# Kernel optimization log

Measured on AMD Instinct MI355X. Metric: run time of the kernel, lower is better.

The kernel has to match this reference:

```python
import jax, jax.numpy as jnp
import numpy as np

N_NODES = 100000
N_EDGES = 1600000
N_GRAPHS = 2000
N_VALUES = 10000
EMB_DIM = 256
N_FEATS = 4


def setup_inputs() -> dict:
    key = jax.random.key(0)
    ks = jax.random.split(key, 7)
    feature = jax.random.randint(ks[0], (N_NODES, N_FEATS), 0, N_VALUES)
    src = jax.random.randint(ks[1], (N_EDGES,), 0, N_NODES)
    dst = jax.random.randint(ks[2], (N_EDGES,), 0, N_NODES)
    graph_ids = jnp.sort(jax.random.randint(ks[3], (N_NODES,), 0, N_GRAPHS))
    emb_table = jax.random.normal(ks[4], (N_VALUES, EMB_DIM), dtype=jnp.float32) * 0.1
    W1 = jax.random.normal(ks[5], (EMB_DIM, EMB_DIM), dtype=jnp.float32) * (EMB_DIM ** -0.5)
    W2 = jax.random.normal(ks[6], (EMB_DIM, EMB_DIM), dtype=jnp.float32) * (EMB_DIM ** -0.5)
    return {"feature": feature, "src": src, "dst": dst, "graph_ids": graph_ids,
            "emb_table": emb_table, "W1": W1, "W2": W2}


def _degree_norms(src, dst, n_nodes):
    ones = jnp.ones(src.shape[0], dtype=jnp.float32)
    out_deg = jax.ops.segment_sum(ones, src, num_segments=n_nodes)
    in_deg = jax.ops.segment_sum(ones, dst, num_segments=n_nodes)
    out_norm = jnp.where(out_deg > 0, jax.lax.rsqrt(jnp.maximum(out_deg, 1.0)), 0.0)[:, None]
    in_norm = jnp.where(in_deg > 0, jax.lax.rsqrt(jnp.maximum(in_deg, 1.0)), 0.0)[:, None]
    return out_norm, in_norm


def _gcn_layer(h, src, dst, out_norm, in_norm, W=None):
    # DGL GraphConv, norm='both', no bias: D_out^{-1/2} scaling, (optional) weight,
    # copy-src/sum aggregation, D_in^{-1/2} scaling.
    h = h * out_norm
    if W is not None:
        h = h @ W
    agg = jax.ops.segment_sum(h[src], dst, num_segments=h.shape[0])  # [N, D]
    return agg * in_norm


def reference(feature, src, dst, graph_ids, emb_table, W1, W2):
    # Embedding lookup + sum over per-node feature slots: [N, F, D] -> [N, D]
    h = jnp.sum(emb_table[feature], axis=1)
    out_norm, in_norm = _degree_norms(src, dst, h.shape[0])
    # layer 0: weight=False
    h = _gcn_layer(h, src, dst, out_norm, in_norm, W=None)
    h = jax.nn.relu(h)
    # layer 1: with weight
    h = _gcn_layer(h, src, dst, out_norm, in_norm, W=W1)
    h = jax.nn.relu(h)
    # final layer: with weight, no relu
    h = _gcn_layer(h, src, dst, out_norm, in_norm, W=W2)
    # sum pooling per graph
    graph_embedding = jax.ops.segment_sum(h, graph_ids, num_segments=N_GRAPHS)
    return graph_embedding
```

## Files before the change

### kernel.cpp

```cpp
#include <hip/hip_runtime.h>
#include <hip/hip_fp16.h>

#define NN 100000
#define NE 1600000
#define NG 2000
#define DIM 256
#define NF 4
#define SCAN_B 1024
#define NBLK ((NN + SCAN_B - 1) / SCAN_B)
#define SCAT_BLK 2048
#define WCONV_BLK 128
#define EMB_BLK ((NN * 64) / 256)

using half8 = __attribute__((ext_vector_type(8))) _Float16;
using f32x4 = __attribute__((ext_vector_type(4))) float;

__device__ inline float4 h4_to_f4(uint2 v) {
    __half2 a = *reinterpret_cast<__half2*>(&v.x);
    __half2 b = *reinterpret_cast<__half2*>(&v.y);
    float2 fa = __half22float2(a);
    float2 fb = __half22float2(b);
    return make_float4(fa.x, fa.y, fb.x, fb.y);
}

__device__ inline uint2 f4_to_h4(float4 r) {
    __half2 a = __floats2half2_rn(r.x, r.y);
    __half2 b = __floats2half2_rn(r.z, r.w);
    uint2 o;
    o.x = *reinterpret_cast<uint*>(&a);
    o.y = *reinterpret_cast<uint*>(&b);
    return o;
}

__device__ inline void add8(float4& a0, float4& a1, uint4 u) {
    uint2 lo2; lo2.x = u.x; lo2.y = u.y;
    uint2 hi2; hi2.x = u.z; hi2.y = u.w;
    float4 lo = h4_to_f4(lo2);
    float4 hi = h4_to_f4(hi2);
    a0.x += lo.x; a0.y += lo.y; a0.z += lo.z; a0.w += lo.w;
    a1.x += hi.x; a1.y += hi.y; a1.z += hi.z; a1.w += hi.w;
}

__global__ void k_count(const int* __restrict__ src, const int* __restrict__ dst,
                        int* __restrict__ outd, int* __restrict__ ind,
                        ushort* __restrict__ slots) {
    int i = blockIdx.x * blockDim.x + threadIdx.x;
    int stride = gridDim.x * blockDim.x;
    for (; i < NE; i += stride) {
        atomicAdd(&outd[src[i]], 1);
        int s = atomicAdd(&ind[dst[i]], 1);
        slots[i] = (ushort)s;
    }
}

__global__ __launch_bounds__(1024) void k_scan1(const int* __restrict__ deg,
                                                int* __restrict__ locex,
                                                int* __restrict__ partials) {
    __shared__ int sm[SCAN_B];
    int t = threadIdx.x;
    int i = blockIdx.x * SCAN_B + t;
    int v = (i < NN) ? deg[i] : 0;
    sm[t] = v;
    __syncthreads();
    for (int off = 1; off < SCAN_B; off <<= 1) {
        int u = (t >= off) ? sm[t - off] : 0;
        __syncthreads();
        sm[t] += u;
        __syncthreads();
    }
    if (i < NN) locex[i] = sm[t] - v;
    if (t == SCAN_B - 1) partials[blockIdx.x] = sm[t];
}

__global__ __launch_bounds__(128) void k_scan2(int* __restrict__ partials,
                                               int* __restrict__ rowptr_last) {
    __shared__ int sm[128];
    int t = threadIdx.x;
    int v = (t < NBLK) ? partials[t] : 0;
    sm[t] = v;
    __syncthreads();
    for (int off = 1; off < 128; off <<= 1) {
        int u = (t >= off) ? sm[t - off] : 0;
        __syncthreads();
        sm[t] += u;
        __syncthreads();
    }
    if (t < NBLK) partials[t] = sm[t] - v;
    if (t == 127) *rowptr_last = sm[127];
}

__global__ __launch_bounds__(1024) void k_scan3(const int* __restrict__ locex,
                                                const int* __restrict__ partials,
                                                const int* __restrict__ outd,
                                                const int* __restrict__ ind,
                                                int* __restrict__ rowptr,
                                                float* __restrict__ onorm,
                                                float* __restrict__ inorm) {
    int i = blockIdx.x * SCAN_B + threadIdx.x;
    if (i < NN) {
        rowptr[i] = locex[i] + partials[blockIdx.x];
        int od = outd[i];
        int id = ind[i];
        onorm[i] = od > 0 ? rsqrtf((float)od) : 0.f;
        inorm[i] = id > 0 ? rsqrtf((float)id) : 0.f;
    }
}

__global__ void k_scatter_wconv_embed(const int* __restrict__ src, const int* __restrict__ dst,
                                      const int* __restrict__ rowptr,
                                      const ushort* __restrict__ slots,
                                      int* __restrict__ col,
                                      const float* __restrict__ W1,
                                      ushort* __restrict__ Wt1,
                                      const int* __restrict__ feat, const float* __restrict__ emb,
                                      const float* __restrict__ onorm, ushort* __restrict__ h) {
    int tid = threadIdx.x;
    if (blockIdx.x < SCAT_BLK) {
        int i = blockIdx.x * 256 + tid;
        const int stride = SCAT_BLK * 256;
        for (; i < NE; i += stride) {
            int d = dst[i];
            col[rowptr[d] + (int)slots[i]] = src[i];
        }
    } else if (blockIdx.x < SCAT_BLK + WCONV_BLK) {
        int idx = (blockIdx.x - SCAT_BLK) * 512 + tid * 2;
        int k0 = idx >> 8;
        int n0 = idx & 255;
        reinterpret_cast<__fp16*>(Wt1)[n0 * DIM + k0] = (__fp16)W1[idx];
        int idx1 = idx + 1;
        int k1 = idx1 >> 8;
        int n1 = idx1 & 255;
        reinterpret_cast<__fp16*>(Wt1)[n1 * DIM + k1] = (__fp16)W1[idx1];
    } else {
        int idx = (blockIdx.x - SCAT_BLK - WCONV_BLK) * 256 + tid;
        int node = idx >> 6;
        int g = idx & 63;
        if (node >= NN) return;
        const int4 f = *reinterpret_cast<const int4*>(feat + node * 4);
        const float4* emb4 = reinterpret_cast<const float4*>(emb);
        float4 a = emb4[(long)f.x * 64 + g];
        float4 b = emb4[(long)f.y * 64 + g];
        float4 c = emb4[(long)f.z * 64 + g];
        float4 d = emb4[(long)f.w * 64 + g];
        float sc = onorm[node];
        float4 r;
        r.x = (a.x + b.x + c.x + d.x) * sc;
        r.y = (a.y + b.y + c.y + d.y) * sc;
        r.z = (a.z + b.z + c.z + d.z) * sc;
        r.w = (a.w + b.w + c.w + d.w) * sc;
        reinterpret_cast<uint2*>(h)[(long)node * 64 + g] = f4_to_h4(r);
    }
}

template <int MODE>
__global__ void k_agg(const int* __restrict__ rowptr, const int* __restrict__ col,
                      const ushort* __restrict__ hin, const float* __restrict__ inorm,
                      const float* __restrict__ onorm, ushort* __restrict__ hout) {
    int wid = (blockIdx.x * blockDim.x + threadIdx.x) >> 6;
    int lane = threadIdx.x & 63;
    if (wid >= NN) return;
    int half = lane >> 5;
    int l32 = lane & 31;
    int e0 = rowptr[wid];
    int e1 = rowptr[wid + 1];
    const uint4* hin4 = reinterpret_cast<const uint4*>(hin);
    float4 aA0 = {0,0,0,0}, aA1 = {0,0,0,0};
    float4 aB0 = {0,0,0,0}, aB1 = {0,0,0,0};
    int e = e0;
    for (; e + 8 <= e1; e += 8) {
        int s0 = col[e + 0 + half];
        int s1 = col[e + 2 + half];
        int s2 = col[e + 4 + half];
        int s3 = col[e + 6 + half];
        uint4 u0 = hin4[(long)s0 * 32 + l32];
        uint4 u1 = hin4[(long)s1 * 32 + l32];
        uint4 u2 = hin4[(long)s2 * 32 + l32];
        uint4 u3 = hin4[(long)s3 * 32 + l32];
        add8(aA0, aA1, u0);
        add8(aB0, aB1, u1);
        add8(aA0, aA1, u2);
        add8(aB0, aB1, u3);
    }
    for (; e < e1; e += 2) {
        int idx = e + half;
        if (idx < e1) {
            int s = col[idx];
            uint4 u = hin4[(long)s * 32 + l32];
            add8(aA0, aA1, u);
        }
    }
    float f[8];
    f[0] = aA0.x + aB0.x; f[1] = aA0.y + aB0.y; f[2] = aA0.z + aB0.z; f[3] = aA0.w + aB0.w;
    f[4] = aA1.x + aB1.x; f[5] = aA1.y + aB1.y; f[6] = aA1.z + aB1.z; f[7] = aA1.w + aB1.w;
#pragma unroll
    for (int j = 0; j < 8; ++j) f[j] += __shfl_xor(f[j], 32);

    float sc = inorm[wid];
    float4 r0, r1;
    if (MODE == 0) {
        float on = onorm[wid];
        r0.x = fmaxf(f[0] * sc, 0.f) * on;
        r0.y = fmaxf(f[1] * sc, 0.f) * on;
        r0.z = fmaxf(f[2] * sc, 0.f) * on;
        r0.w = fmaxf(f[3] * sc, 0.f) * on;
        r1.x = fmaxf(f[4] * sc, 0.f) * on;
        r1.y = fmaxf(f[5] * sc, 0.f) * on;
        r1.z = fmaxf(f[6] * sc, 0.f) * on;
        r1.w = fmaxf(f[7] * sc, 0.f) * on;
    } else {
        r0.x = f[0] * sc; r0.y = f[1] * sc; r0.z = f[2] * sc; r0.w = f[3] * sc;
        r1.x = f[4] * sc; r1.y = f[5] * sc; r1.z = f[6] * sc; r1.w = f[7] * sc;
    }
    if (half == 0) {
        uint2 lo = f4_to_h4(r0);
        uint2 hi = f4_to_h4(r1);
        uint4 o; o.x = lo.x; o.y = lo.y; o.z = hi.x; o.w = hi.y;
        reinterpret_cast<uint4*>(hout)[(long)wid * 32 + l32] = o;
    }
}

__global__ __launch_bounds__(512, 2) void k_gemm(const ushort* __restrict__ x,
                                                 const ushort* __restrict__ Wt,
                                                 ushort* __restrict__ y) {
    __shared__ char wl[131072];
    int tid = threadIdx.x;
    const uint4* Wt4 = reinterpret_cast<const uint4*>(Wt);
#pragma unroll
    for (int it = 0; it < 16; ++it) {
        int chunk = it * 512 + tid;
        int n = chunk >> 5;
        int c16 = chunk & 31;
        uint4 v = Wt4[chunk];
        int off = ((n << 9) + (c16 << 4)) ^ ((n & 7) << 4);
        *reinterpret_cast<uint4*>(&wl[off]) = v;
    }
    __syncthreads();

    int w = tid >> 6;
    int l = tid & 63;
    int wrow = blockIdx.x * 384 + w * 48;
    int lrow = l & 15;
    int lk = l >> 4;

    f32x4 acc[3][16];
#pragma unroll
    for (int m = 0; m < 3; ++m)
#pragma unroll
        for (int n = 0; n < 16; ++n) acc[m][n] = {0.f, 0.f, 0.f, 0.f};

    const char* xb = reinterpret_cast<const char*>(x);
    int r0 = wrow + lrow;
    int r1 = r0 + 16;
    int r2 = r0 + 32;
    r0 = r0 < NN ? r0 : NN - 1;
    r1 = r1 < NN ? r1 : NN - 1;
    r2 = r2 < NN ? r2 : NN - 1;

#pragma unroll
    for (int ks = 0; ks < DIM; ks += 32) {
        long kbyte = (long)(ks + lk * 8) * 2;
        half8 a0 = *reinterpret_cast<const half8*>(xb + (long)r0 * 512 + kbyte);
        half8 a1 = *reinterpret_cast<const half8*>(xb + (long)r1 * 512 + kbyte);
        half8 a2 = *reinterpret_cast<const half8*>(xb + (long)r2 * 512 + kbyte);
#pragma unroll
        for (int fn = 0; fn < 16; ++fn) {
            int n = fn * 16 + lrow;
            int off = ((n << 9) + (int)kbyte) ^ ((n & 7) << 4);
            half8 b = *reinterpret_cast<const half8*>(&wl[off]);
            acc[0][fn] = __builtin_amdgcn_mfma_f32_16x16x32_f16(a0, b, acc[0][fn], 0, 0, 0);
            acc[1][fn] = __builtin_amdgcn_mfma_f32_16x16x32_f16(a1, b, acc[1][fn], 0, 0, 0);
            acc[2][fn] = __builtin_amdgcn_mfma_f32_16x16x32_f16(a2, b, acc[2][fn], 0, 0, 0);
        }
    }

    __fp16* yh = reinterpret_cast<__fp16*>(y);
#pragma unroll
    for (int m = 0; m < 3; ++m) {
        int rbase = wrow + m * 16 + lk * 4;
#pragma unroll
        for (int fn = 0; fn < 16; ++fn) {
            int colc = fn * 16 + lrow;
#pragma unroll
            for (int r = 0; r < 4; ++r) {
                int row = rbase + r;
                if (row < NN) yh[(long)row * DIM + colc] = (__fp16)acc[m][fn][r];
            }
        }
    }
}

__device__ inline int lbound(const int* __restrict__ a, int n, int v) {
    int lo = 0, hi = n;
    while (lo < hi) {
        int m = (lo + hi) >> 1;
        if (a[m] < v) lo = m + 1; else hi = m;
    }
    return lo;
}

__global__ __launch_bounds__(256) void k_pool(const ushort* __restrict__ h,
                                              const int* __restrict__ gids,
                                              float* __restrict__ P) {
    int g = blockIdx.x;
    int t = threadIdx.x;
    int lo = lbound(gids, NN, g);
    int hi = lbound(gids, NN, g + 1);
    const __fp16* hh = reinterpret_cast<const __fp16*>(h);
    float acc = 0.f;
    for (int nd = lo; nd < hi; ++nd) acc += (float)hh[(long)nd * DIM + t];
    P[(long)g * DIM + t] = acc;
}

__global__ __launch_bounds__(256) void k_pgemm(const float* __restrict__ P,
                                               const float* __restrict__ W2,
                                               float* __restrict__ out) {
    __shared__ float Pl[8][DIM];
    int t = threadIdx.x;
    int rbase = blockIdx.x * 8;
#pragma unroll
    for (int r = 0; r < 8; ++r) Pl[r][t] = P[(long)(rbase + r) * DIM + t];
    __syncthreads();
    float acc[8];
#pragma unroll
    for (int r = 0; r < 8; ++r) acc[r] = 0.f;
    for (int k = 0; k < DIM; ++k) {
        float w = W2[(long)k * DIM + t];
#pragma unroll
        for (int r = 0; r < 8; ++r) acc[r] += Pl[r][k] * w;
    }
#pragma unroll
    for (int r = 0; r < 8; ++r) out[(long)(rbase + r) * DIM + t] = acc[r];
}

extern "C" void kernel_launch(void* const* d_in, const int* in_sizes, int n_in,
                              void* d_out, int out_size, void* d_ws, size_t ws_size,
                              hipStream_t stream) {
    const int* feature = (const int*)d_in[0];
    const int* src = (const int*)d_in[1];
    const int* dst = (const int*)d_in[2];
    const int* gids = (const int*)d_in[3];
    const float* emb = (const float*)d_in[4];
    const float* W1 = (const float*)d_in[5];
    const float* W2 = (const float*)d_in[6];
    float* out = (float*)d_out;

    char* p = (char*)d_ws;
    ushort* hA = (ushort*)p;            p += (size_t)NN * DIM * 2;
    ushort* hB = (ushort*)p;            p += (size_t)NN * DIM * 2;
    ushort* Wt1 = (ushort*)p;           p += (size_t)DIM * DIM * 2;
    float* onorm = (float*)p;           p += (size_t)NN * 4;
    float* inorm = (float*)p;           p += (size_t)NN * 4;
    int* rowptr = (int*)p;              p += (size_t)(NN + 4) * 4;
    int* colidx = (int*)p;              p += (size_t)NE * 4;
    int* outd = (int*)p;                p += (size_t)NN * 4;
    int* ind = (int*)p;                 p += (size_t)NN * 4;
    int* locex = (int*)p;               p += (size_t)NN * 4;
    int* partials = (int*)p;            p += (size_t)128 * 4;
    ushort* slots = (ushort*)p;         p += (size_t)NE * 2;
    float* Pbuf = (float*)p;            p += (size_t)NG * DIM * 4;

    hipMemsetAsync(outd, 0, (size_t)2 * NN * 4, stream);

    k_count<<<2048, 256, 0, stream>>>(src, dst, outd, ind, slots);
    k_scan1<<<NBLK, SCAN_B, 0, stream>>>(ind, locex, partials);
    k_scan2<<<1, 128, 0, stream>>>(partials, rowptr + NN);
    k_scan3<<<NBLK, SCAN_B, 0, stream>>>(locex, partials, outd, ind, rowptr, onorm, inorm);
    k_scatter_wconv_embed<<<SCAT_BLK + WCONV_BLK + EMB_BLK, 256, 0, stream>>>(
        src, dst, rowptr, slots, colidx, W1, Wt1, feature, emb, onorm, hA);

    const int aggGrid = (NN * 64 + 255) / 256;
    const int gemmGrid = (NN + 383) / 384;
    k_agg<0><<<aggGrid, 256, 0, stream>>>(rowptr, colidx, hA, inorm, onorm, hB);
    k_gemm<<<gemmGrid, 512, 0, stream>>>(hB, Wt1, hA);
    k_agg<0><<<aggGrid, 256, 0, stream>>>(rowptr, colidx, hA, inorm, onorm, hB);
    k_agg<1><<<aggGrid, 256, 0, stream>>>(rowptr, colidx, hB, inorm, onorm, hA);
    k_pool<<<NG, 256, 0, stream>>>(hA, gids, Pbuf);
    k_pgemm<<<NG / 8, 256, 0, stream>>>(Pbuf, W2, out);
}
```

Baseline: 637.6 us.

## Build CSR via two-level bucket sort instead of global atomic counting

Replaces the per-edge global atomic in-degree counting, the three-kernel scan and the slot-based scatter with a bucketed counting sort. Edges are first binned into 196 coarse destination buckets using shared-memory histograms, then each bucket is sorted locally in LDS to produce rowptr, col and inorm. The out-norm computation is folded into the embedding kernel, which removes two kernel launches. The aim is to cut contended global atomics and random global writes. The cost is an extra 8-byte pair buffer pass, and the sort falls back to direct global writes when a bucket overflows LDS.

After: 577.5 us. 1.1x faster.

```diff
diff --git a/kernel.cpp b/kernel.cpp
--- a/kernel.cpp
+++ b/kernel.cpp
@@ -6,11 +6,16 @@
 #define NG 2000
 #define DIM 256
 #define NF 4
-#define SCAN_B 1024
-#define NBLK ((NN + SCAN_B - 1) / SCAN_B)
-#define SCAT_BLK 2048
+#define NBUK 196
+#define BSH 9
+#define BNODES 512
+#define CHUNKS 512
+#define CHUNK_E (NE / CHUNKS)
+#define OUTD_BLK 1024
+#define BH_BLK CHUNKS
 #define WCONV_BLK 128
 #define EMB_BLK ((NN * 64) / 256)
+#define COLBUF_CAP 12288
 
 using half8 = __attribute__((ext_vector_type(8))) _Float16;
 using f32x4 = __attribute__((ext_vector_type(4))) float;
@@ -41,114 +46,169 @@
     a1.x += hi.x; a1.y += hi.y; a1.z += hi.z; a1.w += hi.w;
 }
 
-__global__ void k_count(const int* __restrict__ src, const int* __restrict__ dst,
-                        int* __restrict__ outd, int* __restrict__ ind,
-                        ushort* __restrict__ slots) {
-    int i = blockIdx.x * blockDim.x + threadIdx.x;
-    int stride = gridDim.x * blockDim.x;
-    for (; i < NE; i += stride) {
-        atomicAdd(&outd[src[i]], 1);
-        int s = atomicAdd(&ind[dst[i]], 1);
-        slots[i] = (ushort)s;
-    }
-}
-
-__global__ __launch_bounds__(1024) void k_scan1(const int* __restrict__ deg,
-                                                int* __restrict__ locex,
-                                                int* __restrict__ partials) {
-    __shared__ int sm[SCAN_B];
-    int t = threadIdx.x;
-    int i = blockIdx.x * SCAN_B + t;
-    int v = (i < NN) ? deg[i] : 0;
-    sm[t] = v;
-    __syncthreads();
-    for (int off = 1; off < SCAN_B; off <<= 1) {
-        int u = (t >= off) ? sm[t - off] : 0;
-        __syncthreads();
-        sm[t] += u;
-        __syncthreads();
-    }
-    if (i < NN) locex[i] = sm[t] - v;
-    if (t == SCAN_B - 1) partials[blockIdx.x] = sm[t];
-}
-
-__global__ __launch_bounds__(128) void k_scan2(int* __restrict__ partials,
-                                               int* __restrict__ rowptr_last) {
-    __shared__ int sm[128];
-    int t = threadIdx.x;
-    int v = (t < NBLK) ? partials[t] : 0;
-    sm[t] = v;
-    __syncthreads();
-    for (int off = 1; off < 128; off <<= 1) {
-        int u = (t >= off) ? sm[t - off] : 0;
-        __syncthreads();
-        sm[t] += u;
-        __syncthreads();
-    }
-    if (t < NBLK) partials[t] = sm[t] - v;
-    if (t == 127) *rowptr_last = sm[127];
-}
-
-__global__ __launch_bounds__(1024) void k_scan3(const int* __restrict__ locex,
-                                                const int* __restrict__ partials,
-                                                const int* __restrict__ outd,
-                                                const int* __restrict__ ind,
-                                                int* __restrict__ rowptr,
-                                                float* __restrict__ onorm,
-                                                float* __restrict__ inorm) {
-    int i = blockIdx.x * SCAN_B + threadIdx.x;
-    if (i < NN) {
-        rowptr[i] = locex[i] + partials[blockIdx.x];
-        int od = outd[i];
-        int id = ind[i];
-        onorm[i] = od > 0 ? rsqrtf((float)od) : 0.f;
-        inorm[i] = id > 0 ? rsqrtf((float)id) : 0.f;
-    }
-}
-
-__global__ void k_scatter_wconv_embed(const int* __restrict__ src, const int* __restrict__ dst,
-                                      const int* __restrict__ rowptr,
-                                      const ushort* __restrict__ slots,
-                                      int* __restrict__ col,
-                                      const float* __restrict__ W1,
-                                      ushort* __restrict__ Wt1,
-                                      const int* __restrict__ feat, const float* __restrict__ emb,
-                                      const float* __restrict__ onorm, ushort* __restrict__ h) {
+__global__ void k_hist(const int* __restrict__ src, const int* __restrict__ dst,
+                       int* __restrict__ outd, int* __restrict__ bcnt,
+                       const float* __restrict__ W1, ushort* __restrict__ Wt1) {
     int tid = threadIdx.x;
-    if (blockIdx.x < SCAT_BLK) {
+    if (blockIdx.x < OUTD_BLK) {
         int i = blockIdx.x * 256 + tid;
-        const int stride = SCAT_BLK * 256;
-        for (; i < NE; i += stride) {
-            int d = dst[i];
-            col[rowptr[d] + (int)slots[i]] = src[i];
-        }
-    } else if (blockIdx.x < SCAT_BLK + WCONV_BLK) {
-        int idx = (blockIdx.x - SCAT_BLK) * 512 + tid * 2;
-        int k0 = idx >> 8;
-        int n0 = idx & 255;
+        const int stride = OUTD_BLK * 256;
+        for (; i < NE; i += stride) atomicAdd(&outd[src[i]], 1);
+    } else if (blockIdx.x < OUTD_BLK + BH_BLK) {
+        __shared__ int h[NBUK];
+        int cb = blockIdx.x - OUTD_BLK;
+        int e0 = cb * CHUNK_E;
+        if (tid < NBUK) h[tid] = 0;
+        __syncthreads();
+        for (int e = e0 + tid; e < e0 + CHUNK_E; e += 256)
+            atomicAdd(&h[dst[e] >> BSH], 1);
+        __syncthreads();
+        if (tid < NBUK && h[tid] > 0) atomicAdd(&bcnt[tid], h[tid]);
+    } else {
+        int idx = (blockIdx.x - OUTD_BLK - BH_BLK) * 512 + tid * 2;
+        int k0 = idx >> 8, n0 = idx & 255;
         reinterpret_cast<__fp16*>(Wt1)[n0 * DIM + k0] = (__fp16)W1[idx];
         int idx1 = idx + 1;
-        int k1 = idx1 >> 8;
-        int n1 = idx1 & 255;
+        int k1 = idx1 >> 8, n1 = idx1 & 255;
         reinterpret_cast<__fp16*>(Wt1)[n1 * DIM + k1] = (__fp16)W1[idx1];
+    }
+}
+
+__global__ __launch_bounds__(256) void k_bscan(const int* __restrict__ bcnt,
+                                               int* __restrict__ boff,
+                                               int* __restrict__ gcur) {
+    __shared__ int sm[256];
+    int t = threadIdx.x;
+    int v = (t < NBUK) ? bcnt[t] : 0;
+    sm[t] = v;
+    __syncthreads();
+    for (int off = 1; off < 256; off <<= 1) {
+        int u = (t >= off) ? sm[t - off] : 0;
+        __syncthreads();
+        sm[t] += u;
+        __syncthreads();
+    }
+    if (t < NBUK) {
+        int ex = sm[t] - v;
+        boff[t] = ex;
+        gcur[t] = ex;
+    }
+    if (t == 255) boff[NBUK] = sm[255];
+}
+
+__global__ void k_bscatter_embed(const int* __restrict__ src, const int* __restrict__ dst,
+                                 int* __restrict__ gcur, uint2* __restrict__ pairs,
+                                 const int* __restrict__ feat, const float* __restrict__ emb,
+                                 const int* __restrict__ outd,
+                                 float* __restrict__ onorm, ushort* __restrict__ h) {
+    int tid = threadIdx.x;
+    if (blockIdx.x < CHUNKS) {
+        __shared__ int h1[NBUK];
+        __shared__ int base1[NBUK];
+        __shared__ int cur1[NBUK];
+        int e0 = blockIdx.x * CHUNK_E;
+        if (tid < NBUK) h1[tid] = 0;
+        __syncthreads();
+        for (int e = e0 + tid; e < e0 + CHUNK_E; e += 256)
+            atomicAdd(&h1[dst[e] >> BSH], 1);
+        __syncthreads();
+        if (tid < NBUK) {
+            int c = h1[tid];
+            base1[tid] = (c > 0) ? atomicAdd(&gcur[tid], c) : 0;
+            cur1[tid] = 0;
+        }
+        __syncthreads();
+        for (int e = e0 + tid; e < e0 + CHUNK_E; e += 256) {
+            int d = dst[e];
+            int b = d >> BSH;
+            int r = atomicAdd(&cur1[b], 1);
+            uint2 pr;
+            pr.x = (uint)d;
+            pr.y = (uint)src[e];
+            pairs[base1[b] + r] = pr;
+        }
     } else {
-        int idx = (blockIdx.x - SCAT_BLK - WCONV_BLK) * 256 + tid;
+        int idx = (blockIdx.x - CHUNKS) * 256 + tid;
         int node = idx >> 6;
         int g = idx & 63;
         if (node >= NN) return;
+        int od = outd[node];
+        float sc = od > 0 ? rsqrtf((float)od) : 0.f;
+        if (g == 0) onorm[node] = sc;
         const int4 f = *reinterpret_cast<const int4*>(feat + node * 4);
         const float4* emb4 = reinterpret_cast<const float4*>(emb);
         float4 a = emb4[(long)f.x * 64 + g];
         float4 b = emb4[(long)f.y * 64 + g];
         float4 c = emb4[(long)f.z * 64 + g];
         float4 d = emb4[(long)f.w * 64 + g];
-        float sc = onorm[node];
         float4 r;
         r.x = (a.x + b.x + c.x + d.x) * sc;
         r.y = (a.y + b.y + c.y + d.y) * sc;
         r.z = (a.z + b.z + c.z + d.z) * sc;
         r.w = (a.w + b.w + c.w + d.w) * sc;
         reinterpret_cast<uint2*>(h)[(long)node * 64 + g] = f4_to_h4(r);
+    }
+}
+
+__global__ __launch_bounds__(1024) void k_bsort(const uint2* __restrict__ pairs,
+                                                const int* __restrict__ boff,
+                                                int* __restrict__ col,
+                                                int* __restrict__ rowptr,
+                                                float* __restrict__ inorm) {
+    __shared__ int hist[BNODES];
+    __shared__ int sc[BNODES];
+    __shared__ int ex[BNODES];
+    __shared__ int cur[BNODES];
+    __shared__ int colbuf[COLBUF_CAP];
+    int t = threadIdx.x;
+    int b = blockIdx.x;
+    int o0 = boff[b];
+    int n = boff[b + 1] - o0;
+
+    if (t < BNODES) hist[t] = 0;
+    __syncthreads();
+    for (int i = t; i < n; i += 1024) {
+        uint2 p = pairs[o0 + i];
+        atomicAdd(&hist[p.x & (BNODES - 1)], 1);
+    }
+    __syncthreads();
+    int v = (t < BNODES) ? hist[t] : 0;
+    if (t < BNODES) sc[t] = v;
+    __syncthreads();
+    for (int off = 1; off < BNODES; off <<= 1) {
+        int u = (t < BNODES && t >= off) ? sc[t - off] : 0;
+        __syncthreads();
+        if (t < BNODES) sc[t] += u;
+        __syncthreads();
+    }
+    if (t < BNODES) {
+        ex[t] = sc[t] - v;
+        cur[t] = 0;
+        int node = (b << BSH) + t;
+        if (node < NN) {
+            rowptr[node] = o0 + ex[t];
+            inorm[node] = v > 0 ? rsqrtf((float)v) : 0.f;
+        }
+    }
+    if (b == NBUK - 1 && t == 0) rowptr[NN] = NE;
+    __syncthreads();
+
+    if (n <= COLBUF_CAP) {
+        for (int i = t; i < n; i += 1024) {
+            uint2 p = pairs[o0 + i];
+            int ld = p.x & (BNODES - 1);
+            int r = atomicAdd(&cur[ld], 1);
+            colbuf[ex[ld] + r] = (int)p.y;
+        }
+        __syncthreads();
+        for (int i = t; i < n; i += 1024) col[o0 + i] = colbuf[i];
+    } else {
+        for (int i = t; i < n; i += 1024) {
+            uint2 p = pairs[o0 + i];
+            int ld = p.x & (BNODES - 1);
+            int r = atomicAdd(&cur[ld], 1);
+            col[o0 + ex[ld] + r] = (int)p.y;
+        }
     }
 }
 
@@ -195,21 +255,21 @@
 #pragma unroll
     for (int j = 0; j < 8; ++j) f[j] += __shfl_xor(f[j], 32);
 
-    float sc = inorm[wid];
+    float scn = inorm[wid];
     float4 r0, r1;
     if (MODE == 0) {
         float on = onorm[wid];
-        r0.x = fmaxf(f[0] * sc, 0.f) * on;
-        r0.y = fmaxf(f[1] * sc, 0.f) * on;
-        r0.z = fmaxf(f[2] * sc, 0.f) * on;
-        r0.w = fmaxf(f[3] * sc, 0.f) * on;
-        r1.x = fmaxf(f[4] * sc, 0.f) * on;
-        r1.y = fmaxf(f[5] * sc, 0.f) * on;
-        r1.z = fmaxf(f[6] * sc, 0.f) * on;
-        r1.w = fmaxf(f[7] * sc, 0.f) * on;
+        r0.x = fmaxf(f[0] * scn, 0.f) * on;
+        r0.y = fmaxf(f[1] * scn, 0.f) * on;
+        r0.z = fmaxf(f[2] * scn, 0.f) * on;
+        r0.w = fmaxf(f[3] * scn, 0.f) * on;
+        r1.x = fmaxf(f[4] * scn, 0.f) * on;
+        r1.y = fmaxf(f[5] * scn, 0.f) * on;
+        r1.z = fmaxf(f[6] * scn, 0.f) * on;
+        r1.w = fmaxf(f[7] * scn, 0.f) * on;
     } else {
-        r0.x = f[0] * sc; r0.y = f[1] * sc; r0.z = f[2] * sc; r0.w = f[3] * sc;
-        r1.x = f[4] * sc; r1.y = f[5] * sc; r1.z = f[6] * sc; r1.w = f[7] * sc;
+        r0.x = f[0] * scn; r0.y = f[1] * scn; r0.z = f[2] * scn; r0.w = f[3] * scn;
+        r1.x = f[4] * scn; r1.y = f[5] * scn; r1.z = f[6] * scn; r1.w = f[7] * scn;
     }
     if (half == 0) {
         uint2 lo = f4_to_h4(r0);
@@ -266,10 +326,10 @@
         for (int fn = 0; fn < 16; ++fn) {
             int n = fn * 16 + lrow;
             int off = ((n << 9) + (int)kbyte) ^ ((n & 7) << 4);
-            half8 b = *reinterpret_cast<const half8*>(&wl[off]);
-            acc[0][fn] = __builtin_amdgcn_mfma_f32_16x16x32_f16(a0, b, acc[0][fn], 0, 0, 0);
-            acc[1][fn] = __builtin_amdgcn_mfma_f32_16x16x32_f16(a1, b, acc[1][fn], 0, 0, 0);
-            acc[2][fn] = __builtin_amdgcn_mfma_f32_16x16x32_f16(a2, b, acc[2][fn], 0, 0, 0);
+            half8 bb = *reinterpret_cast<const half8*>(&wl[off]);
+            acc[0][fn] = __builtin_amdgcn_mfma_f32_16x16x32_f16(a0, bb, acc[0][fn], 0, 0, 0);
+            acc[1][fn] = __builtin_amdgcn_mfma_f32_16x16x32_f16(a1, bb, acc[1][fn], 0, 0, 0);
+            acc[2][fn] = __builtin_amdgcn_mfma_f32_16x16x32_f16(a2, bb, acc[2][fn], 0, 0, 0);
         }
     }
 
@@ -353,20 +413,19 @@
     int* rowptr = (int*)p;              p += (size_t)(NN + 4) * 4;
     int* colidx = (int*)p;              p += (size_t)NE * 4;
     int* outd = (int*)p;                p += (size_t)NN * 4;
-    int* ind = (int*)p;                 p += (size_t)NN * 4;
-    int* locex = (int*)p;               p += (size_t)NN * 4;
-    int* partials = (int*)p;            p += (size_t)128 * 4;
-    ushort* slots = (ushort*)p;         p += (size_t)NE * 2;
+    int* bcnt = (int*)p;                p += (size_t)NBUK * 4;
+    int* boff = (int*)p;                p += (size_t)(NBUK + 4) * 4;
+    int* gcur = (int*)p;                p += (size_t)NBUK * 4;
+    uint2* pairs = (uint2*)p;           p += (size_t)NE * 8;
     float* Pbuf = (float*)p;            p += (size_t)NG * DIM * 4;
 
-    hipMemsetAsync(outd, 0, (size_t)2 * NN * 4, stream);
-
-    k_count<<<2048, 256, 0, stream>>>(src, dst, outd, ind, slots);
-    k_scan1<<<NBLK, SCAN_B, 0, stream>>>(ind, locex, partials);
-    k_scan2<<<1, 128, 0, stream>>>(partials, rowptr + NN);
-    k_scan3<<<NBLK, SCAN_B, 0, stream>>>(locex, partials, outd, ind, rowptr, onorm, inorm);
-    k_scatter_wconv_embed<<<SCAT_BLK + WCONV_BLK + EMB_BLK, 256, 0, stream>>>(
-        src, dst, rowptr, slots, colidx, W1, Wt1, feature, emb, onorm, hA);
+    hipMemsetAsync(outd, 0, (size_t)NN * 4 + (size_t)NBUK * 4, stream);
+
+    k_hist<<<OUTD_BLK + BH_BLK + WCONV_BLK, 256, 0, stream>>>(src, dst, outd, bcnt, W1, Wt1);
+    k_bscan<<<1, 256, 0, stream>>>(bcnt, boff, gcur);
+    k_bscatter_embed<<<CHUNKS + EMB_BLK, 256, 0, stream>>>(src, dst, gcur, pairs,
+                                                           feature, emb, outd, onorm, hA);
+    k_bsort<<<NBUK, 1024, 0, stream>>>(pairs, boff, colidx, rowptr, inorm);
 
     const int aggGrid = (NN * 64 + 255) / 256;
     const int gemmGrid = (NN + 383) / 384;
```
